# Optimization experiments

Hardware: AMD Instinct MI355X
Metric: run time of the kernel (lower is better)

## Reference

```python
import jax, jax.numpy as jnp
import numpy as np

B, HEAD, IMG, STRIDE, C = 8, 512, 1280, 32, 20
FMP = IMG // STRIDE            # 40
N = FMP * FMP                  # 1600 grid cells
CONF_T, NMS_T = 0.001, 0.6


def setup_inputs() -> dict:
    key = jax.random.key(0)
    ks = jax.random.split(key, 8)
    s3 = 1.0 / np.sqrt(HEAD * 9)   # fan-in scaled 3x3 weights
    s1 = 1.0 / np.sqrt(HEAD)
    return {
        "x": jax.random.normal(ks[0], (B, HEAD, FMP, FMP), jnp.float32),
        "cls_w": jax.random.normal(ks[1], (2, HEAD, HEAD, 3, 3), jnp.float32) * s3,
        "cls_b": jnp.zeros((2, HEAD), jnp.float32),
        "reg_w": jax.random.normal(ks[2], (4, HEAD, HEAD, 3, 3), jnp.float32) * s3,
        "reg_b": jnp.zeros((4, HEAD), jnp.float32),
        "obj_w": jax.random.normal(ks[3], (1, HEAD, 1, 1), jnp.float32) * s1,
        "obj_b": jnp.zeros((1,), jnp.float32),
        "clsp_w": jax.random.normal(ks[4], (C, HEAD, 1, 1), jnp.float32) * s1,
        "clsp_b": jnp.zeros((C,), jnp.float32),
        "regp_w": jax.random.normal(ks[5], (4, HEAD, 1, 1), jnp.float32) * s1,
        "regp_b": jnp.zeros((4,), jnp.float32),
    }


def _conv(x, w, b, pad):
    y = jax.lax.conv_general_dilated(
        x, w, (1, 1), [(pad, pad), (pad, pad)],
        dimension_numbers=("NCHW", "OIHW", "NCHW"))
    return y + b[None, :, None, None]


def _leaky(v):
    return jnp.where(v > 0, v, 0.1 * v)


def _head(x, cls_w, cls_b, reg_w, reg_b, obj_w, obj_b, clsp_w, clsp_b, regp_w, regp_b):
    cf = x
    for i in range(2):
        cf = _leaky(_conv(cf, cls_w[i], cls_b[i], 1))
    rf = x
    for i in range(4):
        rf = _leaky(_conv(rf, reg_w[i], reg_b[i], 1))
    b = x.shape[0]
    obj = _conv(rf, obj_w, obj_b, 0).reshape(b, 1, N).transpose(0, 2, 1)   # [B,N,1]
    cls = _conv(cf, clsp_w, clsp_b, 0).reshape(b, C, N).transpose(0, 2, 1) # [B,N,C]
    reg = _conv(rf, regp_w, regp_b, 0).reshape(b, 4, N).transpose(0, 2, 1) # [B,N,4]
    # decode_bbox (center_sample=False)
    gy, gx = jnp.meshgrid(jnp.arange(FMP), jnp.arange(FMP), indexing="ij")
    grid = jnp.stack([gx, gy], -1).reshape(N, 2).astype(jnp.float32)       # [N,2]
    xy = jax.nn.sigmoid(reg[..., :2]) + grid
    wh = jnp.exp(reg[..., 2:])
    box = jnp.concatenate([xy - wh * 0.5, xy + wh * 0.5], -1) * STRIDE     # [B,N,4]
    bboxes = jnp.clip(box / IMG, 0.0, 1.0)
    scores = jax.nn.sigmoid(obj) * jax.nn.softmax(cls, axis=-1)            # [B,N,C]
    return bboxes, scores


def _nms_mask(iou, scores, mask):
    # greedy NMS over boxes where mask is True; returns bool keep mask [N]
    order = jnp.argsort(-jnp.where(mask, scores, -jnp.inf))
    rank = jnp.argsort(order)  # rank[j] = position of box j in score order
    def body(i, keep):
        idx = order[i]
        sup = (iou[idx] > NMS_T) & keep[idx] & (rank > i)
        return keep & ~sup
    return jax.lax.fori_loop(0, scores.shape[0], body, mask)


def _post_one(boxes, scores):
    # boxes [N,4], scores [N,C] -> per-image postprocess
    cls_inds = jnp.argmax(scores, axis=1)
    best = jnp.take_along_axis(scores, cls_inds[:, None], axis=1)[:, 0]
    conf = best >= CONF_T
    x1, y1, x2, y2 = boxes[:, 0], boxes[:, 1], boxes[:, 2], boxes[:, 3]
    areas = (x2 - x1) * (y2 - y1)
    xx1 = jnp.maximum(x1[:, None], x1[None, :])
    yy1 = jnp.maximum(y1[:, None], y1[None, :])
    xx2 = jnp.minimum(x2[:, None], x2[None, :])
    yy2 = jnp.minimum(y2[:, None], y2[None, :])
    w = jnp.maximum(1e-28, xx2 - xx1)
    h = jnp.maximum(1e-28, yy2 - yy1)
    inter = w * h
    iou = inter / (areas[:, None] + areas[None, :] - inter + 1e-14)  # [N,N]
    keep_c = jax.vmap(
        lambda c: _nms_mask(iou, best, conf & (cls_inds == c)))(jnp.arange(C))
    return best, cls_inds.astype(jnp.int32), keep_c.any(0)


def reference(x, cls_w, cls_b, reg_w, reg_b, obj_w, obj_b,
              clsp_w, clsp_b, regp_w, regp_b):
    bboxes, scores = _head(x, cls_w, cls_b, reg_w, reg_b,
                           obj_w, obj_b, clsp_w, clsp_b, regp_w, regp_b)
    best, cls_inds, keep = jax.vmap(_post_one)(bboxes, scores)
    # fixed-shape outputs: boxes [B,N,4], best score [B,N], class id [B,N], keep mask [B,N]
    return bboxes, best, cls_inds, keep
```

## Files before the change

### kernel.cpp

```cpp
#include <hip/hip_runtime.h>
#include <math.h>

#define CH    512
#define FMPX  40
#define PW    42
#define PADN  1764
#define NP    1600
#define BATCH 8
#define NCLS  20
#define CONF_THR 0.001f
#define NMS_THR  0.6f

typedef _Float16 v8h __attribute__((ext_vector_type(8)));
typedef float    v4f __attribute__((ext_vector_type(4)));

#define FPLANE  ((size_t)BATCH * PADN * CH)
#define WSZ     ((size_t)9 * CH * CH)

__device__ __forceinline__ int padidx(int p) { return p + 2 * (p / FMPX) + PW + 1; }

typedef __attribute__((address_space(1))) const void* gas_t;
typedef __attribute__((address_space(3))) void*       las_t;
__device__ __forceinline__ void gl2lds16(const void* g, void* l) {
    __builtin_amdgcn_global_load_lds((gas_t)g, (las_t)l, 16, 0, 0);
}
__device__ __forceinline__ unsigned lds_addr(void* p) {
    return (unsigned)(uintptr_t)(las_t)p;
}
__device__ __forceinline__ v8h lds_b128(unsigned a) {
    v8h r;
    asm volatile("ds_read_b128 %0, %1" : "=v"(r) : "v"(a));
    return r;
}

__global__ __launch_bounds__(256)
void border_zero(uint4* __restrict__ ws) {
    int idx = blockIdx.x * 256 + threadIdx.x;
    int u    = idx & 63;
    int cell = (idx >> 6) % 164;
    int b    = (idx / (64 * 164)) & 7;
    int pl   = idx / (64 * 164 * 8);
    int pi;
    if (cell < 42)      pi = cell;
    else if (cell < 84) pi = 41 * PW + (cell - 42);
    else { int r = cell - 84; pi = (1 + (r >> 1)) * PW + ((r & 1) ? 41 : 0); }
    size_t hoff = (size_t)pl * FPLANE + (size_t)b * (PADN * CH) + (size_t)pi * CH;
    ws[(hoff >> 3) + u] = make_uint4(0u, 0u, 0u, 0u);
}

__global__ __launch_bounds__(256)
void xprep_kernel(const float* __restrict__ x, _Float16* __restrict__ Xh,
                  _Float16* __restrict__ Xl) {
    __shared__ float T[64][65];
    const int t = threadIdx.x;
    const int p0  = blockIdx.x * 64;
    const int ci0 = blockIdx.y * 64;
    const int b   = blockIdx.z;
#pragma unroll
    for (int it = 0; it < 16; ++it) {
        int row = (t >> 6) + 4 * it;
        int col = t & 63;
        T[col][row] = x[((size_t)b * CH + ci0 + row) * NP + p0 + col];
    }
    __syncthreads();
#pragma unroll
    for (int it = 0; it < 16; ++it) {
        int posl = (t >> 6) + 4 * it;
        int ci   = t & 63;
        float v = T[posl][ci];
        _Float16 h = (_Float16)v;
        _Float16 l = (_Float16)((v - (float)h) * 2048.0f);
        size_t o = (size_t)b * (PADN * CH) + (size_t)padidx(p0 + posl) * CH + ci0 + ci;
        Xh[o] = h; Xl[o] = l;
    }
}

__global__ __launch_bounds__(256)
void wtrans_kernel(const float* __restrict__ w, _Float16* __restrict__ Wh,
                   _Float16* __restrict__ Wl) {
    __shared__ float tile[32][289];
    const int t = threadIdx.x;
    const int co0 = blockIdx.x * 32;
    const int ci0 = blockIdx.y * 32;
#pragma unroll
    for (int g = 0; g < 36; ++g) {
        int l = t + 256 * g;
        int co = l / 288, j = l - co * 288;
        tile[co][j] = w[(size_t)(co0 + co) * 4608 + ci0 * 9 + j];
    }
    __syncthreads();
#pragma unroll
    for (int tap = 0; tap < 9; ++tap) {
#pragma unroll
        for (int cg = 0; cg < 4; ++cg) {
            int co = cg * 8 + (t >> 5);
            int ci = t & 31;
            float v = tile[co][ci * 9 + tap];
            _Float16 h = (_Float16)(16.0f * v);
            _Float16 l = (_Float16)((v - (float)h * 0.0625f) * 32768.0f);
            size_t o = ((size_t)tap * CH + co0 + co) * CH + ci0 + ci;
            Wh[o] = h; Wl[o] = l;
        }
    }
}

__global__ __launch_bounds__(512, 2)
void conv_dual(const _Float16* __restrict__ I0h, const _Float16* __restrict__ I0l,
               const _Float16* __restrict__ W0h, const _Float16* __restrict__ W0l,
               const float* __restrict__ bias0,
               _Float16* __restrict__ O0h, _Float16* __restrict__ O0l,
               const _Float16* __restrict__ I1h, const _Float16* __restrict__ I1l,
               const _Float16* __restrict__ W1h, const _Float16* __restrict__ W1l,
               const float* __restrict__ bias1,
               _Float16* __restrict__ O1h, _Float16* __restrict__ O1l) {
    __shared__ _Float16 sm[73728];
    const int t = threadIdx.x;
    const int w = t >> 6, l = t & 63;
    const int quad = l >> 4, col = l & 15;
    const int ph = w >> 2, cq = w & 3;

    const int bid = blockIdx.x;
    const int b   = bid & 7;
    const int q   = bid >> 3;
    const int cid = q / 26;
    const int r   = q - 26 * cid;
    const int co0 = (r & 1) * 256;
    const int p0  = (r >> 1) * 128;

    const _Float16* Ih = cid ? I1h : I0h;
    const _Float16* Il = cid ? I1l : I0l;
    const _Float16* Wh = cid ? W1h : W0h;
    const _Float16* Wl = cid ? W1l : W0l;
    const float*  bias = cid ? bias1 : bias0;
    _Float16* Oh = cid ? O1h : O0h;
    _Float16* Ol = cid ? O1l : O0l;

    const size_t boff = (size_t)b * (PADN * CH);

    const size_t sA  = boff + (size_t)padidx(p0 + 16 * w + col) * CH + quad * 8;
    const size_t sB0 = (size_t)(co0 + 32 * w + col) * CH + quad * 8;
    const int dA = w * 512 + l * 8;
    const int dB = 8192 + (2 * w) * 512 + l * 8;

    const unsigned smB = lds_addr(sm);
    unsigned aRh[4], aRl[4], bRh[4], bRl[4];
#pragma unroll
    for (int i = 0; i < 4; ++i) {
        aRh[i] = smB + (ph * 4 + i) * 1024 + l * 16;
        aRl[i] = aRh[i] + 8192;
    }
#pragma unroll
    for (int j = 0; j < 4; ++j) {
        bRh[j] = smB + 16384 + (cq * 4 + j) * 1024 + l * 16;
        bRl[j] = bRh[j] + 16384;
    }

    const _Float16 *pAh, *pAl, *pWh, *pWl;
    auto set_stage = [&](int ms) {
        const int tap = ms >> 4, cc = (ms & 15) << 5;
        const int ty  = tap / 3;
        const int tsh = ((ty - 1) * PW + (tap - ty * 3 - 1)) * CH + cc;
        const size_t wo = (size_t)tap * (CH * CH) + cc;
        pAh = Ih + sA + tsh;  pAl = Il + sA + tsh;
        pWh = Wh + wo + sB0;  pWl = Wl + wo + sB0;
    };
    auto stage3a = [&](unsigned nH) {
        _Float16* dst = sm + nH;
        gl2lds16(pAh,           dst + dA);
        gl2lds16(pAl,           dst + 4096 + dA);
        gl2lds16(pWh,           dst + dB);
    };
    auto stage3b = [&](unsigned nH) {
        _Float16* dst = sm + nH;
        gl2lds16(pWh + 16 * CH, dst + dB + 512);
        gl2lds16(pWl,           dst + 8192 + dB);
        gl2lds16(pWl + 16 * CH, dst + 8192 + dB + 512);
    };

    v4f acc1[4][4], acc2[4][4];
#pragma unroll
    for (int i = 0; i < 4; ++i)
#pragma unroll
        for (int j = 0; j < 4; ++j) {
            acc1[i][j] = (v4f){0.f, 0.f, 0.f, 0.f};
            acc2[i][j] = (v4f){0.f, 0.f, 0.f, 0.f};
        }

    set_stage(0); stage3a(0);     stage3b(0);
    set_stage(1); stage3a(24576); stage3b(24576);
    set_stage(2);
    asm volatile("s_waitcnt vmcnt(6)" ::: "memory");
    __builtin_amdgcn_s_barrier();

    unsigned c0H = 0, c1H = 24576, c2H = 49152;

#pragma unroll 1
    for (int m = 0; m < 144; ++m) {
        const unsigned bufB = c0H * 2;

        v8h ah[4], al[4], bh[4], bl[4];
#pragma unroll
        for (int i = 0; i < 4; ++i) {
            ah[i] = lds_b128(aRh[i] + bufB);
            al[i] = lds_b128(aRl[i] + bufB);
        }
        bh[0] = lds_b128(bRh[0] + bufB);
        bl[0] = lds_b128(bRl[0] + bufB);
        bh[1] = lds_b128(bRh[1] + bufB);
        bl[1] = lds_b128(bRl[1] + bufB);
        bh[2] = lds_b128(bRh[2] + bufB);
        bl[2] = lds_b128(bRl[2] + bufB);
        bh[3] = lds_b128(bRh[3] + bufB);
        bl[3] = lds_b128(bRl[3] + bufB);

        if (m < 142) stage3a(c2H);

        asm volatile("s_waitcnt lgkmcnt(4)" ::: "memory");
        __builtin_amdgcn_sched_barrier(0);
        __builtin_amdgcn_s_setprio(1);
#pragma unroll
        for (int i = 0; i < 4; ++i)
            acc1[i][0] = __builtin_amdgcn_mfma_f32_16x16x32_f16(ah[i], bh[0], acc1[i][0], 0, 0, 0);
#pragma unroll
        for (int i = 0; i < 4; ++i)
            acc1[i][1] = __builtin_amdgcn_mfma_f32_16x16x32_f16(ah[i], bh[1], acc1[i][1], 0, 0, 0);
#pragma unroll
        for (int i = 0; i < 4; ++i)
            acc2[i][0] = __builtin_amdgcn_mfma_f32_16x16x32_f16(ah[i], bl[0], acc2[i][0], 0, 0, 0);
#pragma unroll
        for (int i = 0; i < 4; ++i)
            acc2[i][1] = __builtin_amdgcn_mfma_f32_16x16x32_f16(ah[i], bl[1], acc2[i][1], 0, 0, 0);
#pragma unroll
        for (int i = 0; i < 4; ++i)
            acc2[i][0] = __builtin_amdgcn_mfma_f32_16x16x32_f16(al[i], bh[0], acc2[i][0], 0, 0, 0);
#pragma unroll
        for (int i = 0; i < 4; ++i)
            acc2[i][1] = __builtin_amdgcn_mfma_f32_16x16x32_f16(al[i], bh[1], acc2[i][1], 0, 0, 0);
        __builtin_amdgcn_s_setprio(0);

        if (m < 142) {
            stage3b(c2H);
            const int nxt = m + 3;
            if (nxt < 144) {
                if ((nxt & 15) == 0) set_stage(nxt);
                else { pAh += 32; pAl += 32; pWh += 32; pWl += 32; }
            }
        }

        asm volatile("s_waitcnt lgkmcnt(0)" ::: "memory");
        __builtin_amdgcn_sched_barrier(0);
        __builtin_amdgcn_s_setprio(1);
#pragma unroll
        for (int i = 0; i < 4; ++i)
            acc1[i][2] = __builtin_amdgcn_mfma_f32_16x16x32_f16(ah[i], bh[2], acc1[i][2], 0, 0, 0);
#pragma unroll
        for (int i = 0; i < 4; ++i)
            acc1[i][3] = __builtin_amdgcn_mfma_f32_16x16x32_f16(ah[i], bh[3], acc1[i][3], 0, 0, 0);
#pragma unroll
        for (int i = 0; i < 4; ++i)
            acc2[i][2] = __builtin_amdgcn_mfma_f32_16x16x32_f16(ah[i], bl[2], acc2[i][2], 0, 0, 0);
#pragma unroll
        for (int i = 0; i < 4; ++i)
            acc2[i][3] = __builtin_amdgcn_mfma_f32_16x16x32_f16(ah[i], bl[3], acc2[i][3], 0, 0, 0);
#pragma unroll
        for (int i = 0; i < 4; ++i)
            acc2[i][2] = __builtin_amdgcn_mfma_f32_16x16x32_f16(al[i], bh[2], acc2[i][2], 0, 0, 0);
#pragma unroll
        for (int i = 0; i < 4; ++i)
            acc2[i][3] = __builtin_amdgcn_mfma_f32_16x16x32_f16(al[i], bh[3], acc2[i][3], 0, 0, 0);
        __builtin_amdgcn_s_setprio(0);

        if (m < 142) {
            asm volatile("s_waitcnt vmcnt(6)" ::: "memory");
            __builtin_amdgcn_s_barrier();
        } else if (m == 142) {
            asm volatile("s_waitcnt vmcnt(0)" ::: "memory");
            __builtin_amdgcn_s_barrier();
        }
        unsigned tmp = c0H; c0H = c1H; c1H = c2H; c2H = tmp;
    }

#pragma unroll
    for (int i = 0; i < 4; ++i) {
#pragma unroll
        for (int j = 0; j < 4; ++j) {
            int n = co0 + cq * 64 + j * 16 + col;
            float bv = bias[n];
#pragma unroll
            for (int rr = 0; rr < 4; ++rr) {
                int p = p0 + ph * 64 + i * 16 + quad * 4 + rr;
                if (p < NP) {
                    float v = acc1[i][j][rr] * 0.0625f + acc2[i][j][rr] * (1.0f / 32768.0f) + bv;
                    v = v > 0.f ? v : 0.1f * v;
                    _Float16 h = (_Float16)v;
                    _Float16 lo = (_Float16)((v - (float)h) * 2048.0f);
                    size_t o = boff + (size_t)padidx(p) * CH + n;
                    Oh[o] = h; Ol[o] = lo;
                }
            }
        }
    }
}

__global__ __launch_bounds__(256)
void head_kernel(const _Float16* __restrict__ Rh, const _Float16* __restrict__ Rl,
                 const _Float16* __restrict__ Ch, const _Float16* __restrict__ Cl,
                 const float* __restrict__ objw, const float* __restrict__ objb,
                 const float* __restrict__ clsw, const float* __restrict__ clsb,
                 const float* __restrict__ regw, const float* __restrict__ regb,
                 float* __restrict__ out) {
    const int wid = (blockIdx.x * 256 + threadIdx.x) >> 6;
    const int l = threadIdx.x & 63;
    const int b = wid / NP, p = wid - b * NP;
    const size_t base = (size_t)b * (PADN * CH) + (size_t)padidx(p) * CH + l * 8;

    v8h rh = *(const v8h*)(Rh + base), rl = *(const v8h*)(Rl + base);
    v8h ch = *(const v8h*)(Ch + base), cl = *(const v8h*)(Cl + base);
    float rv[8], cv[8];
#pragma unroll
    for (int k = 0; k < 8; ++k) {
        rv[k] = (float)rh[k] + (float)rl[k] * (1.0f / 2048.0f);
        cv[k] = (float)ch[k] + (float)cl[k] * (1.0f / 2048.0f);
    }
    float s[25];
#pragma unroll
    for (int o = 0; o < 25; ++o) s[o] = 0.f;
#pragma unroll
    for (int k = 0; k < 8; ++k) s[0] = fmaf(objw[l * 8 + k], rv[k], s[0]);
#pragma unroll
    for (int c = 0; c < NCLS; ++c)
#pragma unroll
        for (int k = 0; k < 8; ++k) s[1 + c] = fmaf(clsw[c * CH + l * 8 + k], cv[k], s[1 + c]);
#pragma unroll
    for (int q = 0; q < 4; ++q)
#pragma unroll
        for (int k = 0; k < 8; ++k) s[21 + q] = fmaf(regw[q * CH + l * 8 + k], rv[k], s[21 + q]);
#pragma unroll
    for (int o = 0; o < 25; ++o) {
#pragma unroll
        for (int off = 32; off > 0; off >>= 1) s[o] += __shfl_xor(s[o], off);
    }
    if (l == 0) {
        int gp = b * NP + p;
        float obj  = s[0] + objb[0];
        float sobj = 1.f / (1.f + expf(-obj));
        float lg[NCLS];
        float m = -1e30f; int am = 0;
#pragma unroll
        for (int c = 0; c < NCLS; ++c) {
            lg[c] = s[1 + c] + clsb[c];
            if (lg[c] > m) { m = lg[c]; am = c; }
        }
        float se = 0.f;
#pragma unroll
        for (int c = 0; c < NCLS; ++c) se += expf(lg[c] - m);
        float best = sobj / se;

        float r0 = s[21] + regb[0], r1 = s[22] + regb[1];
        float r2 = s[23] + regb[2], r3 = s[24] + regb[3];
        int gy = p / FMPX, gx = p - gy * FMPX;
        float cx = 1.f / (1.f + expf(-r0)) + (float)gx;
        float cy = 1.f / (1.f + expf(-r1)) + (float)gy;
        float hw = 0.5f * expf(r2);
        float hh = 0.5f * expf(r3);
        const float sc = 32.f / 1280.f;
        float x1 = fminf(fmaxf((cx - hw) * sc, 0.f), 1.f);
        float y1 = fminf(fmaxf((cy - hh) * sc, 0.f), 1.f);
        float x2 = fminf(fmaxf((cx + hw) * sc, 0.f), 1.f);
        float y2 = fminf(fmaxf((cy + hh) * sc, 0.f), 1.f);

        ((float4*)out)[gp] = make_float4(x1, y1, x2, y2);
        out[4 * BATCH * NP + gp] = best;
        out[5 * BATCH * NP + gp] = (float)am;
        out[6 * BATCH * NP + gp] = 0.f;
    }
}

__global__ __launch_bounds__(1024)
void nms_kernel(float* __restrict__ out) {
    const int c = blockIdx.x, b = blockIdx.y;
    const int t = threadIdx.x;
    const int w = t >> 6, l = t & 63;

    __shared__ unsigned long long skey[2048];
    __shared__ float4 CBox[NP];
    __shared__ float4 KBox[1664];
    __shared__ unsigned long long wmask[16];
    __shared__ int Kcnt;

    for (int j = t; j < NP; j += 1024) {
        int gp = b * NP + j;
        float4 bx = ((const float4*)out)[gp];
        float best = out[4 * BATCH * NP + gp];
        int   ci   = (int)out[5 * BATCH * NP + gp];
        CBox[j] = bx;
        bool alive = (ci == c) && (best >= CONF_THR);
        unsigned long long key = alive
            ? ~(((unsigned long long)__float_as_uint(best) << 32)
                | (unsigned long long)(0xFFFFFFFFu - (unsigned)j))
            : ~0ull;
        skey[j] = key;
    }
    for (int j = NP + t; j < 2048; j += 1024) skey[j] = ~0ull;
    for (int j = t; j < 1664; j += 1024) KBox[j] = make_float4(0.f, 0.f, 0.f, 0.f);
    if (t == 0) Kcnt = 0;

    for (unsigned k = 2; k <= 2048; k <<= 1) {
        for (unsigned j = k >> 1; j > 0; j >>= 1) {
            __syncthreads();
            for (unsigned i = t; i < 2048; i += 1024) {
                unsigned p = i ^ j;
                if (p > i) {
                    bool up = ((i & k) == 0);
                    unsigned long long a = skey[i], bq = skey[p];
                    if ((a > bq) == up) { skey[i] = bq; skey[p] = a; }
                }
            }
        }
    }
    __syncthreads();

    float* keepout = out + 6 * BATCH * NP + b * NP;
    for (int base = 0; base < NP; base += 64) {
        unsigned long long ik = skey[base + l];
        bool valid = (ik != ~0ull);
        unsigned long long vm = __ballot(valid);
        if (vm == 0) break;

        unsigned idx = 0;
        float4 bx = make_float4(0.f, 0.f, 0.f, 0.f);
        float ar = 0.f;
        if (valid) {
            unsigned long long K = ~ik;
            idx = 0xFFFFFFFFu - (unsigned)(K & 0xFFFFFFFFull);
            bx  = CBox[idx];
            ar  = (bx.z - bx.x) * (bx.w - bx.y);
        }
        int prevK = Kcnt;
        int prevKpad = (prevK + 63) & ~63;

        bool sup = false;
        for (int kk = w * 4; kk < prevKpad; kk += 64) {
            float4 kb0 = KBox[kk],     kb1 = KBox[kk + 1];
            float4 kb2 = KBox[kk + 2], kb3 = KBox[kk + 3];
#pragma unroll
            for (int q = 0; q < 4; ++q) {
                float4 kb = q == 0 ? kb0 : q == 1 ? kb1 : q == 2 ? kb2 : kb3;
                float kar = (kb.z - kb.x) * (kb.w - kb.y);
                float xx1 = fmaxf(kb.x, bx.x);
                float yy1 = fmaxf(kb.y, bx.y);
                float xx2 = fminf(kb.z, bx.z);
                float yy2 = fminf(kb.w, bx.w);
                float ww = fmaxf(1e-28f, xx2 - xx1);
                float hh = fmaxf(1e-28f, yy2 - yy1);
                float inter = ww * hh;
                float iou = inter / (kar + ar - inter + 1e-14f);
                sup |= (iou > NMS_THR);
            }
        }
        wmask[w] = __ballot(valid && !sup);
        __syncthreads();

        if (w == 0) {
            unsigned long long alive = wmask[0];
#pragma unroll
            for (int q = 1; q < 16; ++q) alive &= wmask[q];
            unsigned long long smask = 0;
            for (int s = 0; s < 63; ++s) {
                float ox1 = __shfl(bx.x, s), oy1 = __shfl(bx.y, s);
                float ox2 = __shfl(bx.z, s), oy2 = __shfl(bx.w, s);
                float oar = (ox2 - ox1) * (oy2 - oy1);
                float xx1 = fmaxf(ox1, bx.x);
                float yy1 = fmaxf(oy1, bx.y);
                float xx2 = fminf(ox2, bx.z);
                float yy2 = fminf(oy2, bx.w);
                float ww = fmaxf(1e-28f, xx2 - xx1);
                float hh = fmaxf(1e-28f, yy2 - yy1);
                float inter = ww * hh;
                float iou = inter / (oar + ar - inter + 1e-14f);
                if (s < l && iou > NMS_THR) smask |= (1ull << s);
            }
            unsigned long long kept = 0;
            while (alive) {
                int s = __builtin_ctzll(alive);
                kept |= (1ull << s);
                alive &= ~(1ull << s);
                unsigned long long dead = __ballot((smask >> s) & 1ull);
                alive &= ~dead;
            }
            if ((kept >> l) & 1ull) {
                int pos = prevK + __builtin_popcountll(kept & ((1ull << l) - 1ull));
                KBox[pos] = bx;
                keepout[idx] = 1.0f;
            }
            if (l == 0) Kcnt = prevK + __builtin_popcountll(kept);
        }
        __syncthreads();
    }
}

extern "C" void kernel_launch(void* const* d_in, const int* in_sizes, int n_in,
                              void* d_out, int out_size, void* d_ws, size_t ws_size,
                              hipStream_t stream) {
    const float* x      = (const float*)d_in[0];
    const float* cls_w  = (const float*)d_in[1];
    const float* cls_b  = (const float*)d_in[2];
    const float* reg_w  = (const float*)d_in[3];
    const float* reg_b  = (const float*)d_in[4];
    const float* obj_w  = (const float*)d_in[5];
    const float* obj_b  = (const float*)d_in[6];
    const float* clsp_w = (const float*)d_in[7];
    const float* clsp_b = (const float*)d_in[8];
    const float* regp_w = (const float*)d_in[9];
    const float* regp_b = (const float*)d_in[10];
    float* out = (float*)d_out;

    _Float16* ws = (_Float16*)d_ws;
    _Float16* Xh = ws;
    _Float16* Xl = ws + FPLANE;
    _Float16* Ah = ws + 2 * FPLANE;
    _Float16* Al = ws + 3 * FPLANE;
    _Float16* Bh = ws + 4 * FPLANE;
    _Float16* Bl = ws + 5 * FPLANE;
    _Float16* Ch = ws + 6 * FPLANE;
    _Float16* Cl = ws + 7 * FPLANE;
    _Float16* W0h = ws + 8 * FPLANE;
    _Float16* W0l = W0h + WSZ;
    _Float16* W1h = W0l + WSZ;
    _Float16* W1l = W1h + WSZ;
    const size_t LW = (size_t)CH * CH * 9;

    border_zero<<<dim3(2624), 256, 0, stream>>>((uint4*)d_ws);
    xprep_kernel<<<dim3(25, 8, 8), 256, 0, stream>>>(x, Xh, Xl);

    dim3 wgrid(16, 16), blk(256);

    wtrans_kernel<<<wgrid, blk, 0, stream>>>(cls_w, W0h, W0l);
    wtrans_kernel<<<wgrid, blk, 0, stream>>>(reg_w, W1h, W1l);
    conv_dual<<<dim3(416), 512, 0, stream>>>(Xh, Xl, W0h, W0l, cls_b,      Ah, Al,
                                             Xh, Xl, W1h, W1l, reg_b,      Ch, Cl);
    wtrans_kernel<<<wgrid, blk, 0, stream>>>(cls_w + LW, W0h, W0l);
    wtrans_kernel<<<wgrid, blk, 0, stream>>>(reg_w + LW, W1h, W1l);
    conv_dual<<<dim3(416), 512, 0, stream>>>(Ah, Al, W0h, W0l, cls_b + CH, Bh, Bl,
                                             Ch, Cl, W1h, W1l, reg_b + CH, Xh, Xl);
    wtrans_kernel<<<wgrid, blk, 0, stream>>>(reg_w + 2 * LW, W0h, W0l);
    conv_dual<<<dim3(208), 512, 0, stream>>>(Xh, Xl, W0h, W0l, reg_b + 2 * CH, Ch, Cl,
                                             Xh, Xl, W0h, W0l, reg_b + 2 * CH, Ch, Cl);
    wtrans_kernel<<<wgrid, blk, 0, stream>>>(reg_w + 3 * LW, W0h, W0l);
    conv_dual<<<dim3(208), 512, 0, stream>>>(Ch, Cl, W0h, W0l, reg_b + 3 * CH, Xh, Xl,
                                             Ch, Cl, W0h, W0l, reg_b + 3 * CH, Xh, Xl);

    head_kernel<<<dim3(3200), 256, 0, stream>>>(Xh, Xl, Bh, Bl, obj_w, obj_b,
                                                clsp_w, clsp_b, regp_w, regp_b, out);
    nms_kernel<<<dim3(NCLS, BATCH), 1024, 0, stream>>>(out);
}
```

Baseline: 1.742 ms.

## Prefetch next chunk's LDS fragments during MFMA and merge async stages

Restructures the conv GEMM main loop so the A-high and B fragments for the next chunk are read from LDS while the current chunk's MFMAs still run. It ping-pongs between two A-high register sets and unrolls the loop by two. The six global-to-LDS copies are now issued together once per iteration instead of in two halves. The per-iteration wait becomes vmcnt(0) before the barrier, which may expose global load latency, and the extra live fragment registers raise register pressure.

```diff
diff --git a/kernel.cpp b/kernel.cpp
--- a/kernel.cpp
+++ b/kernel.cpp
@@ -164,14 +164,11 @@
         pAh = Ih + sA + tsh;  pAl = Il + sA + tsh;
         pWh = Wh + wo + sB0;  pWl = Wl + wo + sB0;
     };
-    auto stage3a = [&](unsigned nH) {
+    auto stage6 = [&](unsigned nH) {
         _Float16* dst = sm + nH;
         gl2lds16(pAh,           dst + dA);
         gl2lds16(pAl,           dst + 4096 + dA);
         gl2lds16(pWh,           dst + dB);
-    };
-    auto stage3b = [&](unsigned nH) {
-        _Float16* dst = sm + nH;
         gl2lds16(pWh + 16 * CH, dst + dB + 512);
         gl2lds16(pWl,           dst + 8192 + dB);
         gl2lds16(pWl + 16 * CH, dst + 8192 + dB + 512);
@@ -186,34 +183,37 @@
             acc2[i][j] = (v4f){0.f, 0.f, 0.f, 0.f};
         }
 
-    set_stage(0); stage3a(0);     stage3b(0);
-    set_stage(1); stage3a(24576); stage3b(24576);
+    unsigned c0H = 0, c1H = 24576, c2H = 49152;
+
+    set_stage(0); stage6(0);
+    set_stage(1); stage6(24576);
     set_stage(2);
-    asm volatile("s_waitcnt vmcnt(6)" ::: "memory");
+    asm volatile("s_waitcnt vmcnt(0)" ::: "memory");
     __builtin_amdgcn_s_barrier();
 
-    unsigned c0H = 0, c1H = 24576, c2H = 49152;
-
-#pragma unroll 1
-    for (int m = 0; m < 144; ++m) {
-        const unsigned bufB = c0H * 2;
-
-        v8h ah[4], al[4], bh[4], bl[4];
-#pragma unroll
-        for (int i = 0; i < 4; ++i) {
-            ah[i] = lds_b128(aRh[i] + bufB);
-            al[i] = lds_b128(aRl[i] + bufB);
-        }
-        bh[0] = lds_b128(bRh[0] + bufB);
-        bl[0] = lds_b128(bRl[0] + bufB);
-        bh[1] = lds_b128(bRh[1] + bufB);
-        bl[1] = lds_b128(bRl[1] + bufB);
-        bh[2] = lds_b128(bRh[2] + bufB);
-        bl[2] = lds_b128(bRl[2] + bufB);
-        bh[3] = lds_b128(bRh[3] + bufB);
-        bl[3] = lds_b128(bRl[3] + bufB);
-
-        if (m < 142) stage3a(c2H);
+    v8h ahA[4], ahB[4], al[4], bh[4], bl[4];
+#pragma unroll
+    for (int i = 0; i < 4; ++i) ahA[i] = lds_b128(aRh[i]);
+#pragma unroll
+    for (int j = 0; j < 4; ++j) { bh[j] = lds_b128(bRh[j]); bl[j] = lds_b128(bRl[j]); }
+
+    auto chunk_body = [&](int m, v8h (&ah)[4], v8h (&ahN)[4]) {
+        const unsigned b0 = c0H * 2;
+        const unsigned b1 = c1H * 2;
+
+        al[0] = lds_b128(aRl[0] + b0);
+        al[1] = lds_b128(aRl[1] + b0);
+        al[2] = lds_b128(aRl[2] + b0);
+        al[3] = lds_b128(aRl[3] + b0);
+
+        if (m < 142) {
+            stage6(c2H);
+            const int nx = m + 3;
+            if (nx < 144) {
+                if ((nx & 15) == 0) set_stage(nx);
+                else { pAh += 32; pAl += 32; pWh += 32; pWl += 32; }
+            }
+        }
 
         asm volatile("s_waitcnt lgkmcnt(4)" ::: "memory");
         __builtin_amdgcn_sched_barrier(0);
@@ -226,58 +226,52 @@
             acc1[i][1] = __builtin_amdgcn_mfma_f32_16x16x32_f16(ah[i], bh[1], acc1[i][1], 0, 0, 0);
 #pragma unroll
         for (int i = 0; i < 4; ++i)
-            acc2[i][0] = __builtin_amdgcn_mfma_f32_16x16x32_f16(ah[i], bl[0], acc2[i][0], 0, 0, 0);
-#pragma unroll
-        for (int i = 0; i < 4; ++i)
-            acc2[i][1] = __builtin_amdgcn_mfma_f32_16x16x32_f16(ah[i], bl[1], acc2[i][1], 0, 0, 0);
-#pragma unroll
-        for (int i = 0; i < 4; ++i)
-            acc2[i][0] = __builtin_amdgcn_mfma_f32_16x16x32_f16(al[i], bh[0], acc2[i][0], 0, 0, 0);
-#pragma unroll
-        for (int i = 0; i < 4; ++i)
-            acc2[i][1] = __builtin_amdgcn_mfma_f32_16x16x32_f16(al[i], bh[1], acc2[i][1], 0, 0, 0);
-        __builtin_amdgcn_s_setprio(0);
-
-        if (m < 142) {
-            stage3b(c2H);
-            const int nxt = m + 3;
-            if (nxt < 144) {
-                if ((nxt & 15) == 0) set_stage(nxt);
-                else { pAh += 32; pAl += 32; pWh += 32; pWl += 32; }
-            }
-        }
-
-        asm volatile("s_waitcnt lgkmcnt(0)" ::: "memory");
-        __builtin_amdgcn_sched_barrier(0);
-        __builtin_amdgcn_s_setprio(1);
-#pragma unroll
-        for (int i = 0; i < 4; ++i)
             acc1[i][2] = __builtin_amdgcn_mfma_f32_16x16x32_f16(ah[i], bh[2], acc1[i][2], 0, 0, 0);
 #pragma unroll
         for (int i = 0; i < 4; ++i)
             acc1[i][3] = __builtin_amdgcn_mfma_f32_16x16x32_f16(ah[i], bh[3], acc1[i][3], 0, 0, 0);
-#pragma unroll
-        for (int i = 0; i < 4; ++i)
-            acc2[i][2] = __builtin_amdgcn_mfma_f32_16x16x32_f16(ah[i], bl[2], acc2[i][2], 0, 0, 0);
-#pragma unroll
-        for (int i = 0; i < 4; ++i)
-            acc2[i][3] = __builtin_amdgcn_mfma_f32_16x16x32_f16(ah[i], bl[3], acc2[i][3], 0, 0, 0);
-#pragma unroll
-        for (int i = 0; i < 4; ++i)
-            acc2[i][2] = __builtin_amdgcn_mfma_f32_16x16x32_f16(al[i], bh[2], acc2[i][2], 0, 0, 0);
-#pragma unroll
-        for (int i = 0; i < 4; ++i)
-            acc2[i][3] = __builtin_amdgcn_mfma_f32_16x16x32_f16(al[i], bh[3], acc2[i][3], 0, 0, 0);
         __builtin_amdgcn_s_setprio(0);
-
-        if (m < 142) {
-            asm volatile("s_waitcnt vmcnt(6)" ::: "memory");
-            __builtin_amdgcn_s_barrier();
-        } else if (m == 142) {
+        __builtin_amdgcn_sched_barrier(0);
+
+        if (m < 143) {
+            ahN[0] = lds_b128(aRh[0] + b1);
+            ahN[1] = lds_b128(aRh[1] + b1);
+            ahN[2] = lds_b128(aRh[2] + b1);
+            ahN[3] = lds_b128(aRh[3] + b1);
+        }
+
+        if (m < 143) { asm volatile("s_waitcnt lgkmcnt(4)" ::: "memory"); }
+        else         { asm volatile("s_waitcnt lgkmcnt(0)" ::: "memory"); }
+        __builtin_amdgcn_sched_barrier(0);
+
+#pragma unroll
+        for (int j = 0; j < 4; ++j) {
+            __builtin_amdgcn_s_setprio(1);
+#pragma unroll
+            for (int i = 0; i < 4; ++i)
+                acc2[i][j] = __builtin_amdgcn_mfma_f32_16x16x32_f16(ah[i], bl[j], acc2[i][j], 0, 0, 0);
+#pragma unroll
+            for (int i = 0; i < 4; ++i)
+                acc2[i][j] = __builtin_amdgcn_mfma_f32_16x16x32_f16(al[i], bh[j], acc2[i][j], 0, 0, 0);
+            __builtin_amdgcn_s_setprio(0);
+            __builtin_amdgcn_sched_barrier(0);
+            if (m < 143) {
+                bh[j] = lds_b128(bRh[j] + b1);
+                bl[j] = lds_b128(bRl[j] + b1);
+            }
+        }
+
+        if (m < 143) {
             asm volatile("s_waitcnt vmcnt(0)" ::: "memory");
             __builtin_amdgcn_s_barrier();
         }
         unsigned tmp = c0H; c0H = c1H; c1H = c2H; c2H = tmp;
+    };
+
+#pragma unroll 1
+    for (int mo = 0; mo < 144; mo += 2) {
+        chunk_body(mo,     ahA, ahB);
+        chunk_body(mo + 1, ahB, ahA);
     }
 
 #pragma unroll
```

Measured after the change: 1.923 ms. 1.1x slower.
